# Optimization experiments

Hardware: AMD Instinct MI355X
Metric: run time of the kernel (lower is better)

## Reference

```python
import jax, jax.numpy as jnp
import numpy as np

N_NODES = 100000
IN_CH = 256
OUT_CH = 128
HID = 2 * OUT_CH  # 256
N_EDGES = 1600000


def gcn_conv(x, src, dst, W, b, num_nodes):
    """PyG GCNConv: add self-loops, symmetric deg^-1/2 normalization,
    linear transform, scatter-add aggregation, plus bias."""
    h = x @ W  # [N, F_out]
    loop = jnp.arange(num_nodes, dtype=src.dtype)
    src_f = jnp.concatenate([src, loop])
    dst_f = jnp.concatenate([dst, loop])
    ones = jnp.ones(src_f.shape[0], dtype=h.dtype)
    deg = jax.ops.segment_sum(ones, dst_f, num_segments=num_nodes)
    dis = jnp.where(deg > 0, jax.lax.rsqrt(deg), 0.0)
    norm = dis[src_f] * dis[dst_f]  # [E+N]
    msg = h[src_f] * norm[:, None]  # [E+N, F_out]
    out = jax.ops.segment_sum(msg, dst_f, num_segments=num_nodes)
    return out + b


def setup_inputs() -> dict:
    key = jax.random.key(0)
    ks = jax.random.split(key, 8)
    x = jax.random.normal(ks[0], (N_NODES, IN_CH), dtype=jnp.float32)
    edge_index = jax.random.randint(ks[1], (2, N_EDGES), 0, N_NODES, dtype=jnp.int64 if jax.config.jax_enable_x64 else jnp.int32)
    s1 = 1.0 / np.sqrt(IN_CH)
    s2 = 1.0 / np.sqrt(HID)
    W1 = jax.random.uniform(ks[2], (IN_CH, HID), jnp.float32, -s1, s1)
    b1 = jnp.zeros((HID,), jnp.float32)
    W_mu = jax.random.uniform(ks[3], (HID, OUT_CH), jnp.float32, -s2, s2)
    b_mu = jnp.zeros((OUT_CH,), jnp.float32)
    W_lv = jax.random.uniform(ks[4], (HID, OUT_CH), jnp.float32, -s2, s2)
    b_lv = jnp.zeros((OUT_CH,), jnp.float32)
    return {"x": x, "edge_index": edge_index, "W1": W1, "b1": b1,
            "W_mu": W_mu, "b_mu": b_mu, "W_lv": W_lv, "b_lv": b_lv}


def reference(x, edge_index, W1, b1, W_mu, b_mu, W_lv, b_lv):
    src, dst = edge_index[0], edge_index[1]
    h = jax.nn.relu(gcn_conv(x, src, dst, W1, b1, N_NODES))
    mu = gcn_conv(h, src, dst, W_mu, b_mu, N_NODES)
    logvar = gcn_conv(h, src, dst, W_lv, b_lv, N_NODES)
    return (mu, logvar)
```

## Files before the change

kernel.cpp:

```cpp
#include <hip/hip_runtime.h>
#include <hip/hip_fp16.h>

#define N_NODES 100000
#define E_EDGES 1600000
#define F 256
#define LV_OFF 12800000
#define NBUK 782
#define EPB 8192
#define NBLK_BIN 196

typedef _Float16 half8 __attribute__((ext_vector_type(8)));
typedef _Float16 f16x4 __attribute__((ext_vector_type(4)));
typedef float    f32x4 __attribute__((ext_vector_type(4)));

__global__ void k_zero(int* __restrict__ p, int n) {
    int i = blockIdx.x * 256 + threadIdx.x;
    if (i < n) p[i] = 0;
}

__global__ void k_wprep(const float* __restrict__ W1,
                        const float* __restrict__ Wmu, const float* __restrict__ Wlv,
                        _Float16* __restrict__ Wt1, _Float16* __restrict__ Wtc) {
    int idx = blockIdx.x * 256 + threadIdx.x;
    int n = idx >> 8, k = idx & 255;
    Wt1[n * 256 + k] = (_Float16)W1[k * 256 + n];
    float wc = (n < 128) ? Wmu[k * 128 + n] : Wlv[k * 128 + (n - 128)];
    Wtc[n * 256 + k] = (_Float16)wc;
}

__global__ __launch_bounds__(256) void k_binA(const int* __restrict__ dst,
                                              int* __restrict__ gcnt, int* __restrict__ cbase) {
    __shared__ int h[NBUK];
    int blk = blockIdx.x, tid = threadIdx.x;
    for (int b = tid; b < NBUK; b += 256) h[b] = 0;
    __syncthreads();
    int e0 = blk * EPB, e1 = min(e0 + EPB, E_EDGES);
    for (int e = e0 + tid; e < e1; e += 256) atomicAdd(&h[dst[e] >> 7], 1);
    __syncthreads();
    for (int b = tid; b < NBUK; b += 256) {
        int c = h[b];
        cbase[blk * NBUK + b] = c ? atomicAdd(&gcnt[b], c) : 0;
    }
}

__global__ __launch_bounds__(1024) void k_scan782(const int* __restrict__ gcnt,
                                                  int* __restrict__ gbase) {
    __shared__ int sd[1024];
    int tid = threadIdx.x;
    int v = (tid < NBUK) ? gcnt[tid] : 0;
    sd[tid] = v;
    __syncthreads();
    for (int off = 1; off < 1024; off <<= 1) {
        int t = (tid >= off) ? sd[tid - off] : 0;
        __syncthreads();
        sd[tid] += t;
        __syncthreads();
    }
    if (tid < NBUK) gbase[tid] = sd[tid] - v;
    if (tid == NBUK - 1) gbase[NBUK] = sd[tid];
}

__global__ __launch_bounds__(256) void k_binC(const int* __restrict__ src, const int* __restrict__ dst,
                                              const int* __restrict__ gbase, const int* __restrict__ cbase,
                                              unsigned long long* __restrict__ ebuf) {
    __shared__ int h2[NBUK];
    __shared__ int bs[NBUK];
    int blk = blockIdx.x, tid = threadIdx.x;
    for (int b = tid; b < NBUK; b += 256) {
        h2[b] = 0;
        bs[b] = gbase[b] + cbase[blk * NBUK + b];
    }
    __syncthreads();
    int e0 = blk * EPB, e1 = min(e0 + EPB, E_EDGES);
    for (int e = e0 + tid; e < e1; e += 256) {
        int d = dst[e];
        int b = d >> 7;
        int lr = atomicAdd(&h2[b], 1);
        ebuf[bs[b] + lr] = ((unsigned long long)(unsigned)d << 32) | (unsigned)src[e];
    }
}

__global__ __launch_bounds__(256) void k_binD(const unsigned long long* __restrict__ ebuf,
                                              const int* __restrict__ gbase,
                                              int* __restrict__ csr_src, int* __restrict__ row_off,
                                              float* __restrict__ dis) {
    __shared__ int dh[128], dsc[128], dcur[128];
    int b = blockIdx.x, tid = threadIdx.x;
    if (tid < 128) dh[tid] = 0;
    __syncthreads();
    int s0 = gbase[b], s1 = gbase[b + 1];
    for (int i = s0 + tid; i < s1; i += 256)
        atomicAdd(&dh[(int)(ebuf[i] >> 32) & 127], 1);
    __syncthreads();
    if (tid < 128) dsc[tid] = dh[tid];
    __syncthreads();
    for (int off = 1; off < 128; off <<= 1) {
        int t = 0;
        if (tid < 128 && tid >= off) t = dsc[tid - off];
        __syncthreads();
        if (tid < 128) dsc[tid] += t;
        __syncthreads();
    }
    if (tid < 128) {
        int ex = dsc[tid] - dh[tid];
        dcur[tid] = ex;
        int node = b * 128 + tid;
        if (node < N_NODES) {
            row_off[node] = s0 + ex;
            dis[node] = rsqrtf((float)dh[tid] + 1.0f);
        }
    }
    if (b == 0 && tid == 128) row_off[N_NODES] = E_EDGES;
    __syncthreads();
    for (int i = s0 + tid; i < s1; i += 256) {
        unsigned long long ed = ebuf[i];
        int dl = (int)(ed >> 32) & 127;
        int lr = atomicAdd(&dcur[dl], 1);
        csr_src[s0 + lr] = (int)(ed & 0xFFFFFFFFull);
    }
}

template <typename TA>
__global__ __launch_bounds__(256, 2) void k_gemm(
    const TA* __restrict__ A, const _Float16* __restrict__ Bt,
    const float* __restrict__ dis, _Float16* __restrict__ G, int M)
{
    __shared__ _Float16 Ah[128 * 64];
    __shared__ _Float16 Bh[256 * 64];

    const int tid  = threadIdx.x;
    const int m0   = blockIdx.x * 128;
    const int wave = tid >> 6, lane = tid & 63;
    const int wm   = wave & 1, wn = wave >> 1;
    const int lrow = lane & 15, kgrp = lane >> 4;

    f32x4 acc[4][8];
#pragma unroll
    for (int i = 0; i < 4; i++)
#pragma unroll
        for (int j = 0; j < 8; j++) acc[i][j] = (f32x4){0.f, 0.f, 0.f, 0.f};

    for (int kt = 0; kt < 256; kt += 64) {
        if constexpr (sizeof(TA) == 4) {
            const int sr = tid >> 4, kq = tid & 15;
#pragma unroll
            for (int p = 0; p < 8; ++p) {
                int row = p * 16 + sr;
                int gm = m0 + row; if (gm >= M) gm = M - 1;
                float4 v = *reinterpret_cast<const float4*>((const float*)A + (size_t)gm * F + kt + kq * 4);
                f16x4 h4;
                h4[0] = (_Float16)v.x; h4[1] = (_Float16)v.y;
                h4[2] = (_Float16)v.z; h4[3] = (_Float16)v.w;
                *reinterpret_cast<f16x4*>(&Ah[row * 64 + ((kq * 4) ^ ((row & 7) << 3))]) = h4;
            }
        } else {
#pragma unroll
            for (int p = 0; p < 4; ++p) {
                int u = p * 256 + tid;
                int row = u >> 3, slot = u & 7;
                int gm = m0 + row; if (gm >= M) gm = M - 1;
                half8 v = *reinterpret_cast<const half8*>((const _Float16*)A + (size_t)gm * F + kt + slot * 8);
                *reinterpret_cast<half8*>(&Ah[row * 64 + ((slot * 8) ^ ((row & 7) << 3))]) = v;
            }
        }
#pragma unroll
        for (int p = 0; p < 8; ++p) {
            int u = p * 256 + tid;
            int n = u >> 3, slot = u & 7;
            half8 v = *reinterpret_cast<const half8*>(Bt + (size_t)n * F + kt + slot * 8);
            *reinterpret_cast<half8*>(&Bh[n * 64 + ((slot * 8) ^ ((n & 7) << 3))]) = v;
        }
        __syncthreads();
#pragma unroll
        for (int ks = 0; ks < 2; ++ks) {
            int kk = ks * 32 + kgrp * 8;
            half8 ah[4], bh[8];
#pragma unroll
            for (int i = 0; i < 4; ++i) {
                int row = wm * 64 + i * 16 + lrow;
                ah[i] = *reinterpret_cast<const half8*>(&Ah[row * 64 + (kk ^ ((row & 7) << 3))]);
            }
#pragma unroll
            for (int j = 0; j < 8; ++j) {
                int col = wn * 128 + j * 16 + lrow;
                bh[j] = *reinterpret_cast<const half8*>(&Bh[col * 64 + (kk ^ ((col & 7) << 3))]);
            }
#pragma unroll
            for (int i = 0; i < 4; ++i)
#pragma unroll
                for (int j = 0; j < 8; ++j)
                    acc[i][j] = __builtin_amdgcn_mfma_f32_16x16x32_f16(ah[i], bh[j], acc[i][j], 0, 0, 0);
        }
        __syncthreads();
    }

#pragma unroll
    for (int i = 0; i < 4; ++i) {
#pragma unroll
        for (int r = 0; r < 4; ++r) {
            int m = m0 + wm * 64 + i * 16 + kgrp * 4 + r;
            if (m >= M) continue;
            float dv = dis[m];
#pragma unroll
            for (int j = 0; j < 8; ++j) {
                int n = wn * 128 + j * 16 + lrow;
                G[(size_t)m * F + n] = (_Float16)(acc[i][j][r] * dv);
            }
        }
    }
}

__global__ __launch_bounds__(256) void k_aggregate_relu(
    const _Float16* __restrict__ g, const int* __restrict__ row_off,
    const int* __restrict__ csr_src, const float* __restrict__ dis,
    const float* __restrict__ b, _Float16* __restrict__ h)
{
    int d = blockIdx.x * 4 + (threadIdx.x >> 6);
    int lane = threadIdx.x & 63;
    int hf = lane >> 5, lp = lane & 31;
    const half8* g8 = reinterpret_cast<const half8*>(g);
    float a[8] = {0,0,0,0,0,0,0,0}, a2[8] = {0,0,0,0,0,0,0,0};
    float a3[8] = {0,0,0,0,0,0,0,0}, a4[8] = {0,0,0,0,0,0,0,0};
    if (hf == 0) {
        half8 sv = g8[(size_t)d * 32 + lp];
#pragma unroll
        for (int k = 0; k < 8; k++) a[k] = (float)sv[k];
    }
    int j0 = row_off[d], j1 = row_off[d + 1];
    int j = j0 + hf;
    for (; j + 6 < j1; j += 8) {
        int s0 = csr_src[j], s1 = csr_src[j + 2], s2 = csr_src[j + 4], s3 = csr_src[j + 6];
        half8 v0 = g8[(size_t)s0 * 32 + lp];
        half8 v1 = g8[(size_t)s1 * 32 + lp];
        half8 v2 = g8[(size_t)s2 * 32 + lp];
        half8 v3 = g8[(size_t)s3 * 32 + lp];
#pragma unroll
        for (int k = 0; k < 8; k++) {
            a[k] += (float)v0[k]; a2[k] += (float)v1[k];
            a3[k] += (float)v2[k]; a4[k] += (float)v3[k];
        }
    }
    for (; j < j1; j += 2) {
        int s0 = csr_src[j];
        half8 v0 = g8[(size_t)s0 * 32 + lp];
#pragma unroll
        for (int k = 0; k < 8; k++) a[k] += (float)v0[k];
    }
#pragma unroll
    for (int k = 0; k < 8; k++) {
        a[k] += a2[k] + a3[k] + a4[k];
        a[k] += __shfl_xor(a[k], 32);
    }
    float sc = dis[d];
    int c = lp * 8 + hf * 4;
    float4 bb = *reinterpret_cast<const float4*>(b + c);
    f16x4 o;
    o[0] = (_Float16)fmaxf(fmaf(sc, a[hf * 4 + 0], bb.x), 0.0f);
    o[1] = (_Float16)fmaxf(fmaf(sc, a[hf * 4 + 1], bb.y), 0.0f);
    o[2] = (_Float16)fmaxf(fmaf(sc, a[hf * 4 + 2], bb.z), 0.0f);
    o[3] = (_Float16)fmaxf(fmaf(sc, a[hf * 4 + 3], bb.w), 0.0f);
    *reinterpret_cast<f16x4*>(h + (size_t)d * F + c) = o;
}

__global__ __launch_bounds__(256) void k_aggregate_out(
    const _Float16* __restrict__ g, const int* __restrict__ row_off,
    const int* __restrict__ csr_src, const float* __restrict__ dis,
    const float* __restrict__ bmu, const float* __restrict__ blv,
    float* __restrict__ out)
{
    int d = blockIdx.x * 4 + (threadIdx.x >> 6);
    int lane = threadIdx.x & 63;
    int hf = lane >> 5, lp = lane & 31;
    const half8* g8 = reinterpret_cast<const half8*>(g);
    float a[8] = {0,0,0,0,0,0,0,0}, a2[8] = {0,0,0,0,0,0,0,0};
    float a3[8] = {0,0,0,0,0,0,0,0}, a4[8] = {0,0,0,0,0,0,0,0};
    if (hf == 0) {
        half8 sv = g8[(size_t)d * 32 + lp];
#pragma unroll
        for (int k = 0; k < 8; k++) a[k] = (float)sv[k];
    }
    int j0 = row_off[d], j1 = row_off[d + 1];
    int j = j0 + hf;
    for (; j + 6 < j1; j += 8) {
        int s0 = csr_src[j], s1 = csr_src[j + 2], s2 = csr_src[j + 4], s3 = csr_src[j + 6];
        half8 v0 = g8[(size_t)s0 * 32 + lp];
        half8 v1 = g8[(size_t)s1 * 32 + lp];
        half8 v2 = g8[(size_t)s2 * 32 + lp];
        half8 v3 = g8[(size_t)s3 * 32 + lp];
#pragma unroll
        for (int k = 0; k < 8; k++) {
            a[k] += (float)v0[k]; a2[k] += (float)v1[k];
            a3[k] += (float)v2[k]; a4[k] += (float)v3[k];
        }
    }
    for (; j < j1; j += 2) {
        int s0 = csr_src[j];
        half8 v0 = g8[(size_t)s0 * 32 + lp];
#pragma unroll
        for (int k = 0; k < 8; k++) a[k] += (float)v0[k];
    }
#pragma unroll
    for (int k = 0; k < 8; k++) {
        a[k] += a2[k] + a3[k] + a4[k];
        a[k] += __shfl_xor(a[k], 32);
    }
    float sc = dis[d];
    int ch = lp * 8 + hf * 4;
    float va = a[hf * 4 + 0], vb = a[hf * 4 + 1], vc = a[hf * 4 + 2], vd = a[hf * 4 + 3];
    if (ch < 128) {
        float4 bb = *reinterpret_cast<const float4*>(bmu + ch);
        float4 o = make_float4(fmaf(sc, va, bb.x), fmaf(sc, vb, bb.y),
                               fmaf(sc, vc, bb.z), fmaf(sc, vd, bb.w));
        *reinterpret_cast<float4*>(out + (size_t)d * 128 + ch) = o;
    } else {
        int c2 = ch - 128;
        float4 bb = *reinterpret_cast<const float4*>(blv + c2);
        float4 o = make_float4(fmaf(sc, va, bb.x), fmaf(sc, vb, bb.y),
                               fmaf(sc, vc, bb.z), fmaf(sc, vd, bb.w));
        *reinterpret_cast<float4*>(out + LV_OFF + (size_t)d * 128 + c2) = o;
    }
}

extern "C" void kernel_launch(void* const* d_in, const int* in_sizes, int n_in,
                              void* d_out, int out_size, void* d_ws, size_t ws_size,
                              hipStream_t stream) {
    const float* x   = (const float*)d_in[0];
    const int*   ei  = (const int*)d_in[1];
    const int*   src = ei;
    const int*   dst = ei + E_EDGES;
    const float* W1  = (const float*)d_in[2];
    const float* b1  = (const float*)d_in[3];
    const float* Wmu = (const float*)d_in[4];
    const float* bmu = (const float*)d_in[5];
    const float* Wlv = (const float*)d_in[6];
    const float* blv = (const float*)d_in[7];
    float* out = (float*)d_out;

    char* ws = (char*)d_ws;
    size_t o = 0;
    auto carve = [&](size_t bytes) -> char* {
        char* p = ws + o;
        o = (o + bytes + 1023) & ~(size_t)1023;
        return p;
    };
    float*    dis     = (float*)   carve(400000);
    int*      row_off = (int*)     carve(400004);
    int*      gcnt    = (int*)     carve(NBUK * 4);
    int*      gbase   = (int*)     carve((NBUK + 1) * 4);
    int*      cbase   = (int*)     carve((size_t)NBLK_BIN * NBUK * 4);
    _Float16* Wt1     = (_Float16*)carve(131072);
    _Float16* Wtc     = (_Float16*)carve(131072);
    int*      csr_src = (int*)     carve((size_t)E_EDGES * 4);
    unsigned long long* ebuf = (unsigned long long*)carve((size_t)E_EDGES * 8);
    _Float16* g       = (_Float16*)carve((size_t)N_NODES * F * 2);
    (void)ws_size;

    _Float16* h16 = (_Float16*)(out + LV_OFF);

    k_zero   <<<(NBUK + 255) / 256, 256, 0, stream>>>(gcnt, NBUK);
    k_wprep  <<<256, 256, 0, stream>>>(W1, Wmu, Wlv, Wt1, Wtc);
    k_binA   <<<NBLK_BIN, 256, 0, stream>>>(dst, gcnt, cbase);
    k_scan782<<<1, 1024, 0, stream>>>(gcnt, gbase);
    k_binC   <<<NBLK_BIN, 256, 0, stream>>>(src, dst, gbase, cbase, ebuf);
    k_binD   <<<NBUK, 256, 0, stream>>>(ebuf, gbase, csr_src, row_off, dis);

    k_gemm<float><<<782, 256, 0, stream>>>(x, Wt1, dis, g, N_NODES);
    k_aggregate_relu<<<N_NODES / 4, 256, 0, stream>>>(g, row_off, csr_src, dis, b1, h16);

    k_gemm<_Float16><<<782, 256, 0, stream>>>(h16, Wtc, dis, g, N_NODES);
    k_aggregate_out<<<N_NODES / 4, 256, 0, stream>>>(g, row_off, csr_src, dis, bmu, blv, out);
}
```

Measured before the change: 419.3 us.

## Overlap layer-1 GEMM with edge binning and apply source normalization during gather

Weight prep is merged into the first binning pass. The layer-1 GEMM no longer depends on the degree normalization, so it is interleaved with the binC scatter inside one grid of 980 blocks, with every fifth block doing binning, and runs concurrently with it. Because the GEMM output is no longer prescaled by dis[src], the aggregation kernels now load dis[src] per edge and multiply it in. The gather loop is also unrolled to 8 edges per iteration. The cost is an extra scattered 4-byte load per edge in both aggregations, and the GEMM block now shares its grid with heterogeneous work.

```diff
diff --git a/kernel.cpp b/kernel.cpp
--- a/kernel.cpp
+++ b/kernel.cpp
@@ -18,20 +18,22 @@
     if (i < n) p[i] = 0;
 }
 
-__global__ void k_wprep(const float* __restrict__ W1,
-                        const float* __restrict__ Wmu, const float* __restrict__ Wlv,
-                        _Float16* __restrict__ Wt1, _Float16* __restrict__ Wtc) {
-    int idx = blockIdx.x * 256 + threadIdx.x;
-    int n = idx >> 8, k = idx & 255;
-    Wt1[n * 256 + k] = (_Float16)W1[k * 256 + n];
-    float wc = (n < 128) ? Wmu[k * 128 + n] : Wlv[k * 128 + (n - 128)];
-    Wtc[n * 256 + k] = (_Float16)wc;
-}
-
-__global__ __launch_bounds__(256) void k_binA(const int* __restrict__ dst,
-                                              int* __restrict__ gcnt, int* __restrict__ cbase) {
+__global__ __launch_bounds__(256) void k_wprep_binA(
+    const float* __restrict__ W1, const float* __restrict__ Wmu, const float* __restrict__ Wlv,
+    _Float16* __restrict__ Wt1, _Float16* __restrict__ Wtc,
+    const int* __restrict__ dst, int* __restrict__ gcnt, int* __restrict__ cbase)
+{
     __shared__ int h[NBUK];
-    int blk = blockIdx.x, tid = threadIdx.x;
+    int bid = blockIdx.x, tid = threadIdx.x;
+    if (bid < 256) {
+        int idx = bid * 256 + tid;
+        int n = idx >> 8, k = idx & 255;
+        Wt1[n * 256 + k] = (_Float16)W1[k * 256 + n];
+        float wc = (n < 128) ? Wmu[k * 128 + n] : Wlv[k * 128 + (n - 128)];
+        Wtc[n * 256 + k] = (_Float16)wc;
+        return;
+    }
+    int blk = bid - 256;
     for (int b = tid; b < NBUK; b += 256) h[b] = 0;
     __syncthreads();
     int e0 = blk * EPB, e1 = min(e0 + EPB, E_EDGES);
@@ -58,26 +60,6 @@
     }
     if (tid < NBUK) gbase[tid] = sd[tid] - v;
     if (tid == NBUK - 1) gbase[NBUK] = sd[tid];
-}
-
-__global__ __launch_bounds__(256) void k_binC(const int* __restrict__ src, const int* __restrict__ dst,
-                                              const int* __restrict__ gbase, const int* __restrict__ cbase,
-                                              unsigned long long* __restrict__ ebuf) {
-    __shared__ int h2[NBUK];
-    __shared__ int bs[NBUK];
-    int blk = blockIdx.x, tid = threadIdx.x;
-    for (int b = tid; b < NBUK; b += 256) {
-        h2[b] = 0;
-        bs[b] = gbase[b] + cbase[blk * NBUK + b];
-    }
-    __syncthreads();
-    int e0 = blk * EPB, e1 = min(e0 + EPB, E_EDGES);
-    for (int e = e0 + tid; e < e1; e += 256) {
-        int d = dst[e];
-        int b = d >> 7;
-        int lr = atomicAdd(&h2[b], 1);
-        ebuf[bs[b] + lr] = ((unsigned long long)(unsigned)d << 32) | (unsigned)src[e];
-    }
 }
 
 __global__ __launch_bounds__(256) void k_binD(const unsigned long long* __restrict__ ebuf,
@@ -121,15 +103,10 @@
 }
 
 template <typename TA>
-__global__ __launch_bounds__(256, 2) void k_gemm(
+__device__ __forceinline__ void gemm_tile(
     const TA* __restrict__ A, const _Float16* __restrict__ Bt,
-    const float* __restrict__ dis, _Float16* __restrict__ G, int M)
-{
-    __shared__ _Float16 Ah[128 * 64];
-    __shared__ _Float16 Bh[256 * 64];
-
-    const int tid  = threadIdx.x;
-    const int m0   = blockIdx.x * 128;
+    _Float16* __restrict__ G, int M, int m0, int tid, _Float16* Ah, _Float16* Bh)
+{
     const int wave = tid >> 6, lane = tid & 63;
     const int wm   = wave & 1, wn = wave >> 1;
     const int lrow = lane & 15, kgrp = lane >> 4;
@@ -200,12 +177,136 @@
         for (int r = 0; r < 4; ++r) {
             int m = m0 + wm * 64 + i * 16 + kgrp * 4 + r;
             if (m >= M) continue;
-            float dv = dis[m];
 #pragma unroll
             for (int j = 0; j < 8; ++j) {
                 int n = wn * 128 + j * 16 + lrow;
-                G[(size_t)m * F + n] = (_Float16)(acc[i][j][r] * dv);
-            }
+                G[(size_t)m * F + n] = (_Float16)(acc[i][j][r]);
+            }
+        }
+    }
+}
+
+__global__ __launch_bounds__(256, 2) void k_gemm_binC(
+    const float* __restrict__ A, const _Float16* __restrict__ Bt,
+    _Float16* __restrict__ G, int M,
+    const int* __restrict__ src, const int* __restrict__ dst,
+    const int* __restrict__ gbase, const int* __restrict__ cbase,
+    unsigned long long* __restrict__ ebuf)
+{
+    __shared__ _Float16 smem[128 * 64 + 256 * 64];
+    int bid = blockIdx.x, tid = threadIdx.x;
+    int r5 = bid % 5;
+    if (r5 < 4) {
+        int gid = (bid / 5) * 4 + r5;
+        if (gid < 782)
+            gemm_tile<float>(A, Bt, G, M, gid * 128, tid, smem, smem + 128 * 64);
+        return;
+    }
+    int* h2 = (int*)smem;
+    int* bs = h2 + NBUK;
+    int blk = bid / 5;
+    for (int b = tid; b < NBUK; b += 256) {
+        h2[b] = 0;
+        bs[b] = gbase[b] + cbase[blk * NBUK + b];
+    }
+    __syncthreads();
+    int e0 = blk * EPB, e1 = min(e0 + EPB, E_EDGES);
+    for (int e = e0 + tid; e < e1; e += 256) {
+        int d = dst[e];
+        int b = d >> 7;
+        int lr = atomicAdd(&h2[b], 1);
+        ebuf[bs[b] + lr] = ((unsigned long long)(unsigned)d << 32) | (unsigned)src[e];
+    }
+}
+
+__global__ __launch_bounds__(256, 2) void k_gemm_f16(
+    const _Float16* __restrict__ A, const _Float16* __restrict__ Bt,
+    _Float16* __restrict__ G, int M)
+{
+    __shared__ _Float16 smem[128 * 64 + 256 * 64];
+    gemm_tile<_Float16>(A, Bt, G, M, blockIdx.x * 128, threadIdx.x, smem, smem + 128 * 64);
+}
+
+template <int RELU>
+__device__ __forceinline__ void aggregate_body(
+    const _Float16* __restrict__ g, const int* __restrict__ row_off,
+    const int* __restrict__ csr_src, const float* __restrict__ dis,
+    const float* __restrict__ bmu, const float* __restrict__ blv,
+    _Float16* __restrict__ hout, float* __restrict__ out)
+{
+    int d = blockIdx.x * 4 + (threadIdx.x >> 6);
+    int lane = threadIdx.x & 63;
+    int hf = lane >> 5, lp = lane & 31;
+    const half8* g8 = reinterpret_cast<const half8*>(g);
+    float dd = dis[d];
+    float a0[8] = {0,0,0,0,0,0,0,0}, a1[8] = {0,0,0,0,0,0,0,0};
+    float a2[8] = {0,0,0,0,0,0,0,0}, a3[8] = {0,0,0,0,0,0,0,0};
+    if (hf == 0) {
+        half8 sv = g8[(size_t)d * 32 + lp];
+#pragma unroll
+        for (int k = 0; k < 8; k++) a0[k] = dd * (float)sv[k];
+    }
+    int j0 = row_off[d], j1 = row_off[d + 1];
+    int j = j0 + hf;
+    for (; j + 14 < j1; j += 16) {
+        int s[8]; half8 v[8]; float dv[8];
+#pragma unroll
+        for (int p = 0; p < 8; ++p) s[p] = csr_src[j + 2 * p];
+#pragma unroll
+        for (int p = 0; p < 8; ++p) v[p] = g8[(size_t)s[p] * 32 + lp];
+#pragma unroll
+        for (int p = 0; p < 8; ++p) dv[p] = dis[s[p]];
+#pragma unroll
+        for (int k = 0; k < 8; k++) {
+            a0[k] += dv[0] * (float)v[0][k]; a1[k] += dv[1] * (float)v[1][k];
+            a2[k] += dv[2] * (float)v[2][k]; a3[k] += dv[3] * (float)v[3][k];
+            a0[k] += dv[4] * (float)v[4][k]; a1[k] += dv[5] * (float)v[5][k];
+            a2[k] += dv[6] * (float)v[6][k]; a3[k] += dv[7] * (float)v[7][k];
+        }
+    }
+    for (; j + 2 < j1; j += 4) {
+        int sA = csr_src[j], sB = csr_src[j + 2];
+        half8 vA = g8[(size_t)sA * 32 + lp];
+        half8 vB = g8[(size_t)sB * 32 + lp];
+        float dA = dis[sA], dB = dis[sB];
+#pragma unroll
+        for (int k = 0; k < 8; k++) { a0[k] += dA * (float)vA[k]; a1[k] += dB * (float)vB[k]; }
+    }
+    if (j < j1) {
+        int sA = csr_src[j];
+        half8 vA = g8[(size_t)sA * 32 + lp];
+        float dA = dis[sA];
+#pragma unroll
+        for (int k = 0; k < 8; k++) a0[k] += dA * (float)vA[k];
+    }
+#pragma unroll
+    for (int k = 0; k < 8; k++) {
+        a0[k] += a1[k] + a2[k] + a3[k];
+        a0[k] += __shfl_xor(a0[k], 32);
+    }
+    if (RELU) {
+        int c = lp * 8 + hf * 4;
+        float4 bb = *reinterpret_cast<const float4*>(bmu + c);
+        f16x4 o;
+        o[0] = (_Float16)fmaxf(fmaf(dd, a0[hf * 4 + 0], bb.x), 0.0f);
+        o[1] = (_Float16)fmaxf(fmaf(dd, a0[hf * 4 + 1], bb.y), 0.0f);
+        o[2] = (_Float16)fmaxf(fmaf(dd, a0[hf * 4 + 2], bb.z), 0.0f);
+        o[3] = (_Float16)fmaxf(fmaf(dd, a0[hf * 4 + 3], bb.w), 0.0f);
+        *reinterpret_cast<f16x4*>(hout + (size_t)d * F + c) = o;
+    } else {
+        int ch = lp * 8 + hf * 4;
+        float va = a0[hf * 4 + 0], vb = a0[hf * 4 + 1], vc = a0[hf * 4 + 2], vd = a0[hf * 4 + 3];
+        if (ch < 128) {
+            float4 bb = *reinterpret_cast<const float4*>(bmu + ch);
+            float4 o = make_float4(fmaf(dd, va, bb.x), fmaf(dd, vb, bb.y),
+                                   fmaf(dd, vc, bb.z), fmaf(dd, vd, bb.w));
+            *reinterpret_cast<float4*>(out + (size_t)d * 128 + ch) = o;
+        } else {
+            int c2 = ch - 128;
+            float4 bb = *reinterpret_cast<const float4*>(blv + c2);
+            float4 o = make_float4(fmaf(dd, va, bb.x), fmaf(dd, vb, bb.y),
+                                   fmaf(dd, vc, bb.z), fmaf(dd, vd, bb.w));
+            *reinterpret_cast<float4*>(out + LV_OFF + (size_t)d * 128 + c2) = o;
         }
     }
 }
@@ -215,51 +316,7 @@
     const int* __restrict__ csr_src, const float* __restrict__ dis,
     const float* __restrict__ b, _Float16* __restrict__ h)
 {
-    int d = blockIdx.x * 4 + (threadIdx.x >> 6);
-    int lane = threadIdx.x & 63;
-    int hf = lane >> 5, lp = lane & 31;
-    const half8* g8 = reinterpret_cast<const half8*>(g);
-    float a[8] = {0,0,0,0,0,0,0,0}, a2[8] = {0,0,0,0,0,0,0,0};
-    float a3[8] = {0,0,0,0,0,0,0,0}, a4[8] = {0,0,0,0,0,0,0,0};
-    if (hf == 0) {
-        half8 sv = g8[(size_t)d * 32 + lp];
-#pragma unroll
-        for (int k = 0; k < 8; k++) a[k] = (float)sv[k];
-    }
-    int j0 = row_off[d], j1 = row_off[d + 1];
-    int j = j0 + hf;
-    for (; j + 6 < j1; j += 8) {
-        int s0 = csr_src[j], s1 = csr_src[j + 2], s2 = csr_src[j + 4], s3 = csr_src[j + 6];
-        half8 v0 = g8[(size_t)s0 * 32 + lp];
-        half8 v1 = g8[(size_t)s1 * 32 + lp];
-        half8 v2 = g8[(size_t)s2 * 32 + lp];
-        half8 v3 = g8[(size_t)s3 * 32 + lp];
-#pragma unroll
-        for (int k = 0; k < 8; k++) {
-            a[k] += (float)v0[k]; a2[k] += (float)v1[k];
-            a3[k] += (float)v2[k]; a4[k] += (float)v3[k];
-        }
-    }
-    for (; j < j1; j += 2) {
-        int s0 = csr_src[j];
-        half8 v0 = g8[(size_t)s0 * 32 + lp];
-#pragma unroll
-        for (int k = 0; k < 8; k++) a[k] += (float)v0[k];
-    }
-#pragma unroll
-    for (int k = 0; k < 8; k++) {
-        a[k] += a2[k] + a3[k] + a4[k];
-        a[k] += __shfl_xor(a[k], 32);
-    }
-    float sc = dis[d];
-    int c = lp * 8 + hf * 4;
-    float4 bb = *reinterpret_cast<const float4*>(b + c);
-    f16x4 o;
-    o[0] = (_Float16)fmaxf(fmaf(sc, a[hf * 4 + 0], bb.x), 0.0f);
-    o[1] = (_Float16)fmaxf(fmaf(sc, a[hf * 4 + 1], bb.y), 0.0f);
-    o[2] = (_Float16)fmaxf(fmaf(sc, a[hf * 4 + 2], bb.z), 0.0f);
-    o[3] = (_Float16)fmaxf(fmaf(sc, a[hf * 4 + 3], bb.w), 0.0f);
-    *reinterpret_cast<f16x4*>(h + (size_t)d * F + c) = o;
+    aggregate_body<1>(g, row_off, csr_src, dis, b, nullptr, h, nullptr);
 }
 
 __global__ __launch_bounds__(256) void k_aggregate_out(
@@ -268,57 +325,7 @@
     const float* __restrict__ bmu, const float* __restrict__ blv,
     float* __restrict__ out)
 {
-    int d = blockIdx.x * 4 + (threadIdx.x >> 6);
-    int lane = threadIdx.x & 63;
-    int hf = lane >> 5, lp = lane & 31;
-    const half8* g8 = reinterpret_cast<const half8*>(g);
-    float a[8] = {0,0,0,0,0,0,0,0}, a2[8] = {0,0,0,0,0,0,0,0};
-    float a3[8] = {0,0,0,0,0,0,0,0}, a4[8] = {0,0,0,0,0,0,0,0};
-    if (hf == 0) {
-        half8 sv = g8[(size_t)d * 32 + lp];
-#pragma unroll
-        for (int k = 0; k < 8; k++) a[k] = (float)sv[k];
-    }
-    int j0 = row_off[d], j1 = row_off[d + 1];
-    int j = j0 + hf;
-    for (; j + 6 < j1; j += 8) {
-        int s0 = csr_src[j], s1 = csr_src[j + 2], s2 = csr_src[j + 4], s3 = csr_src[j + 6];
-        half8 v0 = g8[(size_t)s0 * 32 + lp];
-        half8 v1 = g8[(size_t)s1 * 32 + lp];
-        half8 v2 = g8[(size_t)s2 * 32 + lp];
-        half8 v3 = g8[(size_t)s3 * 32 + lp];
-#pragma unroll
-        for (int k = 0; k < 8; k++) {
-            a[k] += (float)v0[k]; a2[k] += (float)v1[k];
-            a3[k] += (float)v2[k]; a4[k] += (float)v3[k];
-        }
-    }
-    for (; j < j1; j += 2) {
-        int s0 = csr_src[j];
-        half8 v0 = g8[(size_t)s0 * 32 + lp];
-#pragma unroll
-        for (int k = 0; k < 8; k++) a[k] += (float)v0[k];
-    }
-#pragma unroll
-    for (int k = 0; k < 8; k++) {
-        a[k] += a2[k] + a3[k] + a4[k];
-        a[k] += __shfl_xor(a[k], 32);
-    }
-    float sc = dis[d];
-    int ch = lp * 8 + hf * 4;
-    float va = a[hf * 4 + 0], vb = a[hf * 4 + 1], vc = a[hf * 4 + 2], vd = a[hf * 4 + 3];
-    if (ch < 128) {
-        float4 bb = *reinterpret_cast<const float4*>(bmu + ch);
-        float4 o = make_float4(fmaf(sc, va, bb.x), fmaf(sc, vb, bb.y),
-                               fmaf(sc, vc, bb.z), fmaf(sc, vd, bb.w));
-        *reinterpret_cast<float4*>(out + (size_t)d * 128 + ch) = o;
-    } else {
-        int c2 = ch - 128;
-        float4 bb = *reinterpret_cast<const float4*>(blv + c2);
-        float4 o = make_float4(fmaf(sc, va, bb.x), fmaf(sc, vb, bb.y),
-                               fmaf(sc, vc, bb.z), fmaf(sc, vd, bb.w));
-        *reinterpret_cast<float4*>(out + LV_OFF + (size_t)d * 128 + c2) = o;
-    }
+    aggregate_body<0>(g, row_off, csr_src, dis, bmu, blv, nullptr, out);
 }
 
 extern "C" void kernel_launch(void* const* d_in, const int* in_sizes, int n_in,
@@ -357,16 +364,14 @@
 
     _Float16* h16 = (_Float16*)(out + LV_OFF);
 
-    k_zero   <<<(NBUK + 255) / 256, 256, 0, stream>>>(gcnt, NBUK);
-    k_wprep  <<<256, 256, 0, stream>>>(W1, Wmu, Wlv, Wt1, Wtc);
-    k_binA   <<<NBLK_BIN, 256, 0, stream>>>(dst, gcnt, cbase);
-    k_scan782<<<1, 1024, 0, stream>>>(gcnt, gbase);
-    k_binC   <<<NBLK_BIN, 256, 0, stream>>>(src, dst, gbase, cbase, ebuf);
-    k_binD   <<<NBUK, 256, 0, stream>>>(ebuf, gbase, csr_src, row_off, dis);
-
-    k_gemm<float><<<782, 256, 0, stream>>>(x, Wt1, dis, g, N_NODES);
+    k_zero      <<<(NBUK + 255) / 256, 256, 0, stream>>>(gcnt, NBUK);
+    k_wprep_binA<<<256 + NBLK_BIN, 256, 0, stream>>>(W1, Wmu, Wlv, Wt1, Wtc, dst, gcnt, cbase);
+    k_scan782   <<<1, 1024, 0, stream>>>(gcnt, gbase);
+    k_gemm_binC <<<980, 256, 0, stream>>>(x, Wt1, g, N_NODES, src, dst, gbase, cbase, ebuf);
+    k_binD      <<<NBUK, 256, 0, stream>>>(ebuf, gbase, csr_src, row_off, dis);
+
     k_aggregate_relu<<<N_NODES / 4, 256, 0, stream>>>(g, row_off, csr_src, dis, b1, h16);
 
-    k_gemm<_Float16><<<782, 256, 0, stream>>>(h16, Wtc, dis, g, N_NODES);
+    k_gemm_f16<<<782, 256, 0, stream>>>(h16, Wtc, g, N_NODES);
     k_aggregate_out<<<N_NODES / 4, 256, 0, stream>>>(g, row_off, csr_src, dis, bmu, blv, out);
 }
```

Result: no change. 422.7 us (+0.8%).
